# Kernel optimization log

Hardware: AMD Instinct MI355X
Metric: run time of the kernel (lower is better)

The kernel has to match this reference:

```python
import jax, jax.numpy as jnp
import numpy as np

N_NODES = 19385
N_EDGES = 1_200_000
GNN = 256
HID = 512
RANK = 512
NCLS = 3
NGENES = 6640
NBLK = 6
B = 256
EPS = 1e-5


def _ln(x, g, b):
    m = jnp.mean(x, axis=-1, keepdims=True)
    v = jnp.mean(jnp.square(x - m), axis=-1, keepdims=True)
    return (x - m) * jax.lax.rsqrt(v + EPS) * g + b


def setup_inputs() -> dict:
    key = jax.random.key(0)
    ks = iter(jax.random.split(key, 40))
    w = lambda shape, s=0.02: jax.random.normal(next(ks), shape, jnp.float32) * s
    inp = {
        'node_idx': jax.random.randint(next(ks), (B,), -1, N_NODES),  # -1 == OOV
        'edge_index': jax.random.randint(next(ks), (2, N_EDGES), 0, N_NODES),
        'edge_weight': jax.random.uniform(next(ks), (N_EDGES,), jnp.float32),
        'frozen_emb': jax.random.normal(next(ks), (N_NODES, GNN), jnp.float32),
        # trainable partial GNN (mps.6, mps.7, post_mp)
        'conv6_W': w((GNN, GNN)), 'conv6_b': jnp.zeros((GNN,)),
        'ln6_g': jnp.ones((GNN,)), 'ln6_b': jnp.zeros((GNN,)),
        'conv7_W': w((GNN, GNN)), 'conv7_b': jnp.zeros((GNN,)),
        'ln7_g': jnp.ones((GNN,)), 'ln7_b': jnp.zeros((GNN,)),
        'post_W': w((GNN, GNN)), 'post_b': jnp.zeros((GNN,)),
        # head
        'oov_emb': w((GNN,)),
        'in_ln_g': jnp.ones((GNN,)), 'in_ln_b': jnp.zeros((GNN,)),
        'proj_in_W': w((GNN, HID)), 'proj_in_b': jnp.zeros((HID,)),
        'rb_ln_g': jnp.ones((NBLK, HID)), 'rb_ln_b': jnp.zeros((NBLK, HID)),
        'rb_W1': w((NBLK, HID, 4 * HID)), 'rb_b1': jnp.zeros((NBLK, 4 * HID)),
        'rb_W2': w((NBLK, 4 * HID, HID)), 'rb_b2': jnp.zeros((NBLK, HID)),
        'out_ln_g': jnp.ones((HID,)), 'out_ln_b': jnp.zeros((HID,)),
        'bil_W': w((HID, NCLS * RANK)), 'bil_b': jnp.zeros((NCLS * RANK,)),
        'out_gene_emb': w((NGENES, RANK)),
    }
    return inp


def reference(node_idx, edge_index, edge_weight, frozen_emb,
              conv6_W, conv6_b, ln6_g, ln6_b,
              conv7_W, conv7_b, ln7_g, ln7_b,
              post_W, post_b,
              oov_emb, in_ln_g, in_ln_b, proj_in_W, proj_in_b,
              rb_ln_g, rb_ln_b, rb_W1, rb_b1, rb_W2, rb_b2,
              out_ln_g, out_ln_b, bil_W, bil_b, out_gene_emb):
    src, dst = edge_index[0], edge_index[1]

    def conv(x, W, b):
        # edge-weighted message passing: gather -> scale -> scatter-add -> linear
        msg = x[src] * edge_weight[:, None]              # [E, GNN]
        agg = jax.ops.segment_sum(msg, dst, num_segments=N_NODES)
        return agg @ W + b

    # trainable GNN layers (eval mode: dropout = identity)
    x = frozen_emb
    x = x + jax.nn.relu(_ln(conv(x, conv6_W, conv6_b), ln6_g, ln6_b))
    x = x + jax.nn.relu(_ln(conv(x, conv7_W, conv7_b), ln7_g, ln7_b))
    node_emb = x @ post_W + post_b                       # [N, GNN]

    # OOV-aware lookup
    in_f = (node_idx >= 0).astype(jnp.float32)[:, None]  # [B,1]
    gnn_emb = node_emb[jnp.clip(node_idx, 0, None)]      # [B, GNN]
    h = gnn_emb * in_f + oov_emb[None, :] * (1.0 - in_f)

    # MLP head
    h = _ln(h, in_ln_g, in_ln_b) @ proj_in_W + proj_in_b
    for i in range(NBLK):
        t = _ln(h, rb_ln_g[i], rb_ln_b[i])
        t = jax.nn.gelu(t @ rb_W1[i] + rb_b1[i])
        h = h + t @ rb_W2[i] + rb_b2[i]
    h = _ln(h, out_ln_g, out_ln_b)

    pert = (h @ bil_W + bil_b).reshape(B, NCLS, RANK)
    logits = jnp.einsum('bcr,gr->bcg', pert, out_gene_emb)  # [B, 3, 6640]
    return logits
```

## Files before the change

### kernel.cpp

```cpp
#include <hip/hip_runtime.h>
#include <hip/hip_bf16.h>
#include <cstdint>
#include <cstddef>

#define N_NODES_C 19385
#define N_EDGES_C 1200000
#define GNN_C 256
#define HID_C 512
#define RANK_C 512
#define NCLS_C 3
#define NGENES_C 6640
#define NBLK_C 6
#define B_C 256
#define LN_EPS 1e-5f

typedef short bf8v __attribute__((ext_vector_type(8)));
typedef float f4v __attribute__((ext_vector_type(4)));

__device__ __forceinline__ float bfu2f(unsigned short u) {
  union { unsigned int i; float f; } c; c.i = ((unsigned)u) << 16; return c.f;
}
__device__ __forceinline__ unsigned short f2bfu(float v) {
  union { float f; unsigned u; } c; c.f = v;
  unsigned r = c.u + 0x7FFFu + ((c.u >> 16) & 1u);
  return (unsigned short)(r >> 16);
}
__device__ __forceinline__ float gelu_tanh(float v) {
  const float x3 = v * v * v;
  return 0.5f * v * (1.f + tanhf(0.7978845608028654f * (v + 0.044715f * x3)));
}


struct CvtSeg { const float* s; unsigned short* d; long long n; };
struct CvtArgs { CvtSeg seg[2]; int nseg; };

__global__ __launch_bounds__(256) void multicvt_kernel(CvtArgs a) {
  for (int sg = 0; sg < a.nseg; ++sg) {
    const float4* s = reinterpret_cast<const float4*>(a.seg[sg].s);
    unsigned short* d = a.seg[sg].d;
    const long long n4 = a.seg[sg].n >> 2;
    for (long long i = blockIdx.x * 256 + threadIdx.x; i < n4;
         i += (long long)gridDim.x * 256) {
      float4 v = s[i];
      ushort4 o;
      o.x = f2bfu(v.x); o.y = f2bfu(v.y); o.z = f2bfu(v.z); o.w = f2bfu(v.w);
      *reinterpret_cast<ushort4*>(d + i * 4) = o;
    }
  }
}


struct TSeg { const float* s; unsigned short* d; int R, C; };
struct TArgs { TSeg seg[12]; int nseg; };

__global__ __launch_bounds__(256) void multitrans_kernel(TArgs a) {
  __shared__ float tile[32][33];
  const int tx = threadIdx.x & 31;
  const int ty = threadIdx.x >> 5;
  for (int sg = 0; sg < a.nseg; ++sg) {
    const int R = a.seg[sg].R, C = a.seg[sg].C;
    const int tC = C >> 5;
    const int nt = (R >> 5) * tC;
    const float* src = a.seg[sg].s;
    unsigned short* dst = a.seg[sg].d;
    for (int tid = blockIdx.x; tid < nt; tid += gridDim.x) {
      const int tr = tid / tC, tc = tid - tr * tC;
      const int r0 = tr * 32, c0 = tc * 32;
      __syncthreads();
#pragma unroll
      for (int j = 0; j < 32; j += 8)
        tile[ty + j][tx] = src[(size_t)(r0 + ty + j) * C + c0 + tx];
      __syncthreads();
#pragma unroll
      for (int j = 0; j < 32; j += 8)
        dst[(size_t)(c0 + ty + j) * R + r0 + tx] = f2bfu(tile[tx][ty + j]);
    }
  }
}


__global__ __launch_bounds__(256) void hist_kernel(const int* __restrict__ dst,
                                                   int* __restrict__ cnt, int E) {
  int i = blockIdx.x * 256 + threadIdx.x;
  if (i < E) atomicAdd(&cnt[dst[i]], 1);
}

__global__ __launch_bounds__(1024) void scan_kernel(const int* __restrict__ cnt,
                                                    int* __restrict__ off, int n) {
  __shared__ int sums[1024];
  const int t = threadIdx.x;
  const int CH = (n + 1023) >> 10;
  const int base = t * CH;
  int s = 0;
  for (int i = 0; i < CH; ++i) {
    int idx = base + i;
    if (idx < n) s += cnt[idx];
  }
  sums[t] = s;
  __syncthreads();
  for (int d = 1; d < 1024; d <<= 1) {
    int v = (t >= d) ? sums[t - d] : 0;
    __syncthreads();
    sums[t] += v;
    __syncthreads();
  }
  int run = (t == 0) ? 0 : sums[t - 1];
  for (int i = 0; i < CH; ++i) {
    int idx = base + i;
    if (idx < n) { off[idx] = run; run += cnt[idx]; }
  }
  if (t == 0) off[n] = sums[1023];
}

__global__ __launch_bounds__(256) void fill_kernel(const int* __restrict__ src,
                                                   const int* __restrict__ dst,
                                                   const float* __restrict__ ew,
                                                   const int* __restrict__ off,
                                                   int* __restrict__ cur,
                                                   int* __restrict__ bsrc,
                                                   float* __restrict__ bw, int E) {
  int i = blockIdx.x * 256 + threadIdx.x;
  if (i < E) {
    int d = dst[i];
    int p = atomicAdd(&cur[d], 1);
    int q = off[d] + p;
    bsrc[q] = src[i] * GNN_C;
    bw[q] = ew[i];
  }
}

__global__ __launch_bounds__(256) void mark_kernel(const int* __restrict__ node_idx,
                                                   const int* __restrict__ off,
                                                   const int* __restrict__ bsrc,
                                                   int* __restrict__ needed) {
  const int b = blockIdx.x;
  const int n = max(node_idx[b], 0);
  if (threadIdx.x == 0) needed[n] = 1;
  const int s0 = off[n], s1 = off[n + 1];
  for (int p = s0 + threadIdx.x; p < s1; p += 256)
    needed[bsrc[p] >> 8] = 1;
}


__global__ __launch_bounds__(256) void agg_full_kernel(const int* __restrict__ bsrc,
                                                       const float* __restrict__ bw,
                                                       const int* __restrict__ off,
                                                       const int* __restrict__ needed,
                                                       const unsigned short* __restrict__ x,
                                                       unsigned short* __restrict__ aggbf) {
  const int n = blockIdx.x;
  if (!needed[n]) return;
  __shared__ f4v red[4][64];
  const int t = threadIdx.x;
  const int w = __builtin_amdgcn_readfirstlane(t >> 6);
  const int lane = t & 63;
  const int s0 = off[n];
  const int c = off[n + 1] - s0;
  const int q0 = s0 + ((c * w) >> 2);
  const int q1 = s0 + ((c * (w + 1)) >> 2);
  float a0 = 0.f, a1 = 0.f, a2 = 0.f, a3 = 0.f;
  const unsigned short* xl = x + 4 * lane;
#pragma unroll 4
  for (int p = q0; p < q1; ++p) {
    const int s = bsrc[p];
    const float wg = bw[p];
    const ushort4 v = *reinterpret_cast<const ushort4*>(xl + s);
    a0 = fmaf(bfu2f(v.x), wg, a0);
    a1 = fmaf(bfu2f(v.y), wg, a1);
    a2 = fmaf(bfu2f(v.z), wg, a2);
    a3 = fmaf(bfu2f(v.w), wg, a3);
  }
  f4v av; av[0] = a0; av[1] = a1; av[2] = a2; av[3] = a3;
  red[w][lane] = av;
  __syncthreads();
  const float* rf = reinterpret_cast<const float*>(red);
  const float sum = rf[t] + rf[256 + t] + rf[512 + t] + rf[768 + t];
  aggbf[(size_t)n * GNN_C + t] = f2bfu(sum);
}

__global__ __launch_bounds__(256) void agg_sel_kernel(const int* __restrict__ node_idx,
                                                      const int* __restrict__ bsrc,
                                                      const float* __restrict__ bw,
                                                      const int* __restrict__ off,
                                                      const float* __restrict__ x,
                                                      unsigned short* __restrict__ aggbf) {
  __shared__ f4v red[4][64];
  const int b = blockIdx.x;
  const int t = threadIdx.x;
  const int n = max(node_idx[b], 0);
  const int w = __builtin_amdgcn_readfirstlane(t >> 6);
  const int lane = t & 63;
  const int s0 = off[n];
  const int c = off[n + 1] - s0;
  const int q0 = s0 + ((c * w) >> 2);
  const int q1 = s0 + ((c * (w + 1)) >> 2);
  float a0 = 0.f, a1 = 0.f, a2 = 0.f, a3 = 0.f;
  const float* xl = x + 4 * lane;
#pragma unroll 2
  for (int p = q0; p < q1; ++p) {
    const int s = bsrc[p];
    const float wg = bw[p];
    const f4v v = *reinterpret_cast<const f4v*>(xl + s);
    a0 = fmaf(v[0], wg, a0);
    a1 = fmaf(v[1], wg, a1);
    a2 = fmaf(v[2], wg, a2);
    a3 = fmaf(v[3], wg, a3);
  }
  f4v av; av[0] = a0; av[1] = a1; av[2] = a2; av[3] = a3;
  red[w][lane] = av;
  __syncthreads();
  const float* rf = reinterpret_cast<const float*>(red);
  const float sum = rf[t] + rf[256 + t] + rf[512 + t] + rf[768 + t];
  aggbf[(size_t)b * GNN_C + t] = f2bfu(sum);
}


#define MBK 32
#define MLDW 40

__global__ __launch_bounds__(256) void mgemm_kernel(const unsigned short* __restrict__ A,
                                                    const unsigned short* __restrict__ Bt,
                                                    const float* __restrict__ bias,
                                                    float* __restrict__ C,
                                                    int M, int N, int K) {
  __shared__ unsigned short As[128][MLDW];
  __shared__ unsigned short Bs[128][MLDW];
  const int t = threadIdx.x;
  const int lane = t & 63;
  const int wave = t >> 6;
  const int r0 = blockIdx.x * 128;
  const int c0 = blockIdx.y * 128;
  const int wm = (wave >> 1) * 64;
  const int wn = (wave & 1) * 64;
  const int lm = lane & 15;
  const int lq = lane >> 4;

  f4v acc[4][4];
  for (int i = 0; i < 4; ++i)
    for (int j = 0; j < 4; ++j)
      for (int r = 0; r < 4; ++r) acc[i][j][r] = 0.f;

  const int row = t >> 1;
  const int kof = (t & 1) * 16;
  for (int k0 = 0; k0 < K; k0 += MBK) {
    {
      const int gr = r0 + row;
      uint4 u0 = make_uint4(0, 0, 0, 0), u1 = u0;
      if (gr < M) {
        const uint4* p = reinterpret_cast<const uint4*>(A + (size_t)gr * K + k0 + kof);
        u0 = p[0]; u1 = p[1];
      }
      *reinterpret_cast<uint4*>(&As[row][kof]) = u0;
      *reinterpret_cast<uint4*>(&As[row][kof + 8]) = u1;
    }
    {
      const int gn = c0 + row;
      uint4 u0 = make_uint4(0, 0, 0, 0), u1 = u0;
      if (gn < N) {
        const uint4* p = reinterpret_cast<const uint4*>(Bt + (size_t)gn * K + k0 + kof);
        u0 = p[0]; u1 = p[1];
      }
      *reinterpret_cast<uint4*>(&Bs[row][kof]) = u0;
      *reinterpret_cast<uint4*>(&Bs[row][kof + 8]) = u1;
    }
    __syncthreads();

    bf8v a[4], b[4];
#pragma unroll
    for (int i = 0; i < 4; ++i)
      a[i] = *reinterpret_cast<const bf8v*>(&As[wm + i * 16 + lm][lq * 8]);
#pragma unroll
    for (int j = 0; j < 4; ++j)
      b[j] = *reinterpret_cast<const bf8v*>(&Bs[wn + j * 16 + lm][lq * 8]);
#pragma unroll
    for (int i = 0; i < 4; ++i)
#pragma unroll
      for (int j = 0; j < 4; ++j)
        acc[i][j] = __builtin_amdgcn_mfma_f32_16x16x32_bf16(a[i], b[j], acc[i][j], 0, 0, 0);
    __syncthreads();
  }

  for (int ti = 0; ti < 4; ++ti) {
    for (int tj = 0; tj < 4; ++tj) {
      const int col = c0 + wn + tj * 16 + lm;
      if (col >= N) continue;
      const float bv = bias ? bias[col] : 0.f;
      for (int r = 0; r < 4; ++r) {
        const int row2 = r0 + wm + ti * 16 + lq * 4 + r;
        if (row2 < M) C[(size_t)row2 * N + col] = acc[ti][tj][r] + bv;
      }
    }
  }
}


__global__ __launch_bounds__(256) void mgemm64_kernel(const unsigned short* __restrict__ A,
                                                      const unsigned short* __restrict__ Bt,
                                                      const float* __restrict__ bias,
                                                      float* outF, unsigned short* outB,
                                                      int M, int N, int K, int doGelu) {
  __shared__ unsigned short As[64][MLDW];
  __shared__ unsigned short Bs[64][MLDW];
  const int t = threadIdx.x;
  const int lane = t & 63;
  const int wave = t >> 6;
  const int r0 = blockIdx.x * 64;
  const int c0 = blockIdx.y * 64;
  const int wm = (wave >> 1) * 32;
  const int wn = (wave & 1) * 32;
  const int lm = lane & 15;
  const int lq = lane >> 4;

  f4v acc[2][2];
  for (int i = 0; i < 2; ++i)
    for (int j = 0; j < 2; ++j)
      for (int r = 0; r < 4; ++r) acc[i][j][r] = 0.f;

  const int row = t >> 2;
  const int kof = (t & 3) * 8;
  for (int k0 = 0; k0 < K; k0 += MBK) {
    *reinterpret_cast<uint4*>(&As[row][kof]) =
        *reinterpret_cast<const uint4*>(A + (size_t)(r0 + row) * K + k0 + kof);
    *reinterpret_cast<uint4*>(&Bs[row][kof]) =
        *reinterpret_cast<const uint4*>(Bt + (size_t)(c0 + row) * K + k0 + kof);
    __syncthreads();
    bf8v a[2], b[2];
#pragma unroll
    for (int i = 0; i < 2; ++i)
      a[i] = *reinterpret_cast<const bf8v*>(&As[wm + i * 16 + lm][lq * 8]);
#pragma unroll
    for (int j = 0; j < 2; ++j)
      b[j] = *reinterpret_cast<const bf8v*>(&Bs[wn + j * 16 + lm][lq * 8]);
#pragma unroll
    for (int i = 0; i < 2; ++i)
#pragma unroll
      for (int j = 0; j < 2; ++j)
        acc[i][j] = __builtin_amdgcn_mfma_f32_16x16x32_bf16(a[i], b[j], acc[i][j], 0, 0, 0);
    __syncthreads();
  }

  for (int ti = 0; ti < 2; ++ti) {
    for (int tj = 0; tj < 2; ++tj) {
      const int col = c0 + wn + tj * 16 + lm;
      const float bv = bias ? bias[col] : 0.f;
      for (int r = 0; r < 4; ++r) {
        const int row2 = r0 + wm + ti * 16 + lq * 4 + r;
        float v = acc[ti][tj][r] + bv;
        if (doGelu) v = gelu_tanh(v);
        if (outF) outF[(size_t)row2 * N + col] = v;
        else outB[(size_t)row2 * N + col] = f2bfu(v);
      }
    }
  }
}

__global__ __launch_bounds__(256) void skmgemm64_kernel(const unsigned short* __restrict__ A,
                                                        const unsigned short* __restrict__ Bt,
                                                        float* __restrict__ part,
                                                        int M, int N, int K, int kc) {
  __shared__ unsigned short As[64][MLDW];
  __shared__ unsigned short Bs[64][MLDW];
  const int t = threadIdx.x;
  const int lane = t & 63;
  const int wave = t >> 6;
  const int r0 = blockIdx.x * 64;
  const int c0 = blockIdx.y * 64;
  const int kBeg = blockIdx.z * kc;
  const int kEnd = kBeg + kc;
  const int wm = (wave >> 1) * 32;
  const int wn = (wave & 1) * 32;
  const int lm = lane & 15;
  const int lq = lane >> 4;

  f4v acc[2][2];
  for (int i = 0; i < 2; ++i)
    for (int j = 0; j < 2; ++j)
      for (int r = 0; r < 4; ++r) acc[i][j][r] = 0.f;

  const int row = t >> 2;
  const int kof = (t & 3) * 8;
  for (int k0 = kBeg; k0 < kEnd; k0 += MBK) {
    *reinterpret_cast<uint4*>(&As[row][kof]) =
        *reinterpret_cast<const uint4*>(A + (size_t)(r0 + row) * K + k0 + kof);
    *reinterpret_cast<uint4*>(&Bs[row][kof]) =
        *reinterpret_cast<const uint4*>(Bt + (size_t)(c0 + row) * K + k0 + kof);
    __syncthreads();
    bf8v a[2], b[2];
#pragma unroll
    for (int i = 0; i < 2; ++i)
      a[i] = *reinterpret_cast<const bf8v*>(&As[wm + i * 16 + lm][lq * 8]);
#pragma unroll
    for (int j = 0; j < 2; ++j)
      b[j] = *reinterpret_cast<const bf8v*>(&Bs[wn + j * 16 + lm][lq * 8]);
#pragma unroll
    for (int i = 0; i < 2; ++i)
#pragma unroll
      for (int j = 0; j < 2; ++j)
        acc[i][j] = __builtin_amdgcn_mfma_f32_16x16x32_bf16(a[i], b[j], acc[i][j], 0, 0, 0);
    __syncthreads();
  }

  float* out = part + (size_t)blockIdx.z * M * N;
  for (int ti = 0; ti < 2; ++ti)
    for (int tj = 0; tj < 2; ++tj) {
      const int col = c0 + wn + tj * 16 + lm;
      for (int r = 0; r < 4; ++r) {
        const int row2 = r0 + wm + ti * 16 + lq * 4 + r;
        out[(size_t)row2 * N + col] = acc[ti][tj][r];
      }
    }
}


__global__ __launch_bounds__(256) void postconv6_kernel(const float* __restrict__ g,
                                                        const float* __restrict__ b,
                                                        const float* __restrict__ frozen,
                                                        const int* __restrict__ needed,
                                                        float* __restrict__ yx) {
  __shared__ float sb[4];
  const int n = blockIdx.x, t = threadIdx.x;
  if (!needed[n]) return;
  const float v = yx[(size_t)n * GNN_C + t];
  float s = v;
  for (int o = 32; o; o >>= 1) s += __shfl_down(s, o, 64);
  if ((t & 63) == 0) sb[t >> 6] = s;
  __syncthreads();
  const float m = (sb[0] + sb[1] + sb[2] + sb[3]) * (1.f / GNN_C);
  __syncthreads();
  const float d = v - m;
  s = d * d;
  for (int o = 32; o; o >>= 1) s += __shfl_down(s, o, 64);
  if ((t & 63) == 0) sb[t >> 6] = s;
  __syncthreads();
  const float rs = rsqrtf((sb[0] + sb[1] + sb[2] + sb[3]) * (1.f / GNN_C) + LN_EPS);
  const float xn = d * rs * g[t] + b[t];
  yx[(size_t)n * GNN_C + t] = frozen[(size_t)n * GNN_C + t] + fmaxf(xn, 0.f);
}

__global__ __launch_bounds__(256) void postconv7_kernel(const float* __restrict__ y,
                                                        const float* __restrict__ g,
                                                        const float* __restrict__ b,
                                                        const int* __restrict__ idx,
                                                        const float* __restrict__ x1f,
                                                        unsigned short* __restrict__ out) {
  __shared__ float sb[4];
  const int bi = blockIdx.x, t = threadIdx.x;
  const int n = max(idx[bi], 0);
  const float v = y[(size_t)bi * GNN_C + t];
  float s = v;
  for (int o = 32; o; o >>= 1) s += __shfl_down(s, o, 64);
  if ((t & 63) == 0) sb[t >> 6] = s;
  __syncthreads();
  const float m = (sb[0] + sb[1] + sb[2] + sb[3]) * (1.f / GNN_C);
  __syncthreads();
  const float d = v - m;
  s = d * d;
  for (int o = 32; o; o >>= 1) s += __shfl_down(s, o, 64);
  if ((t & 63) == 0) sb[t >> 6] = s;
  __syncthreads();
  const float rs = rsqrtf((sb[0] + sb[1] + sb[2] + sb[3]) * (1.f / GNN_C) + LN_EPS);
  const float xn = d * rs * g[t] + b[t];
  out[(size_t)bi * GNN_C + t] = f2bfu(x1f[(size_t)n * GNN_C + t] + fmaxf(xn, 0.f));
}

__global__ __launch_bounds__(256) void h0ln_kernel(const float* __restrict__ ne,
                                                   const int* __restrict__ idx,
                                                   const float* __restrict__ oov,
                                                   const float* __restrict__ g,
                                                   const float* __restrict__ b,
                                                   unsigned short* __restrict__ out) {
  __shared__ float sb[4];
  const int bi = blockIdx.x, t = threadIdx.x;
  const float v = (idx[bi] >= 0) ? ne[(size_t)bi * GNN_C + t] : oov[t];
  float s = v;
  for (int o = 32; o; o >>= 1) s += __shfl_down(s, o, 64);
  if ((t & 63) == 0) sb[t >> 6] = s;
  __syncthreads();
  const float m = (sb[0] + sb[1] + sb[2] + sb[3]) * (1.f / GNN_C);
  __syncthreads();
  const float d = v - m;
  s = d * d;
  for (int o = 32; o; o >>= 1) s += __shfl_down(s, o, 64);
  if ((t & 63) == 0) sb[t >> 6] = s;
  __syncthreads();
  const float rs = rsqrtf((sb[0] + sb[1] + sb[2] + sb[3]) * (1.f / GNN_C) + LN_EPS);
  out[(size_t)bi * GNN_C + t] = f2bfu(d * rs * g[t] + b[t]);
}

__global__ __launch_bounds__(256) void lnbf_kernel(const float* __restrict__ in,
                                                   const float* __restrict__ g,
                                                   const float* __restrict__ b,
                                                   unsigned short* __restrict__ out) {
  __shared__ float sb[4];
  const int r = blockIdx.x, t = threadIdx.x;
  const float v0 = in[(size_t)r * HID_C + t];
  const float v1 = in[(size_t)r * HID_C + t + 256];
  float s = v0 + v1;
  for (int o = 32; o; o >>= 1) s += __shfl_down(s, o, 64);
  if ((t & 63) == 0) sb[t >> 6] = s;
  __syncthreads();
  const float m = (sb[0] + sb[1] + sb[2] + sb[3]) * (1.f / HID_C);
  __syncthreads();
  const float d0 = v0 - m, d1 = v1 - m;
  s = d0 * d0 + d1 * d1;
  for (int o = 32; o; o >>= 1) s += __shfl_down(s, o, 64);
  if ((t & 63) == 0) sb[t >> 6] = s;
  __syncthreads();
  const float rs = rsqrtf((sb[0] + sb[1] + sb[2] + sb[3]) * (1.f / HID_C) + LN_EPS);
  out[(size_t)r * HID_C + t] = f2bfu(d0 * rs * g[t] + b[t]);
  out[(size_t)r * HID_C + t + 256] = f2bfu(d1 * rs * g[t + 256] + b[t + 256]);
}

__global__ __launch_bounds__(256) void combln_kernel(const float* __restrict__ part,
                                                     float* __restrict__ h,
                                                     const float* __restrict__ b2,
                                                     const float* __restrict__ g,
                                                     const float* __restrict__ b,
                                                     unsigned short* __restrict__ out) {
  __shared__ float sb[4];
  const int r = blockIdx.x, t = threadIdx.x;
  const int MN = B_C * HID_C;
  const size_t o0 = (size_t)r * HID_C + t;
  const size_t o1 = o0 + 256;
  float v0 = h[o0] + b2[t] + part[o0] + part[MN + o0] + part[2 * MN + o0] + part[3 * MN + o0];
  float v1 = h[o1] + b2[t + 256] + part[o1] + part[MN + o1] + part[2 * MN + o1] + part[3 * MN + o1];
  h[o0] = v0;
  h[o1] = v1;
  float s = v0 + v1;
  for (int o = 32; o; o >>= 1) s += __shfl_down(s, o, 64);
  if ((t & 63) == 0) sb[t >> 6] = s;
  __syncthreads();
  const float m = (sb[0] + sb[1] + sb[2] + sb[3]) * (1.f / HID_C);
  __syncthreads();
  const float d0 = v0 - m, d1 = v1 - m;
  s = d0 * d0 + d1 * d1;
  for (int o = 32; o; o >>= 1) s += __shfl_down(s, o, 64);
  if ((t & 63) == 0) sb[t >> 6] = s;
  __syncthreads();
  const float rs = rsqrtf((sb[0] + sb[1] + sb[2] + sb[3]) * (1.f / HID_C) + LN_EPS);
  out[o0] = f2bfu(d0 * rs * g[t] + b[t]);
  out[o1] = f2bfu(d1 * rs * g[t + 256] + b[t + 256]);
}


extern "C" void kernel_launch(void* const* d_in, const int* in_sizes, int n_in,
                              void* d_out, int out_size, void* d_ws, size_t ws_size,
                              hipStream_t stream) {
  const int* node_idx = (const int*)d_in[0];
  const int* e_src = (const int*)d_in[1];
  const int* e_dst = e_src + N_EDGES_C;
  const float* ew = (const float*)d_in[2];
  const float* frozen = (const float*)d_in[3];
  const float* W6 = (const float*)d_in[4];
  const float* b6 = (const float*)d_in[5];
  const float* g6 = (const float*)d_in[6];
  const float* bl6 = (const float*)d_in[7];
  const float* W7 = (const float*)d_in[8];
  const float* b7 = (const float*)d_in[9];
  const float* g7 = (const float*)d_in[10];
  const float* bl7 = (const float*)d_in[11];
  const float* postW = (const float*)d_in[12];
  const float* postb = (const float*)d_in[13];
  const float* oov = (const float*)d_in[14];
  const float* ing = (const float*)d_in[15];
  const float* inb = (const float*)d_in[16];
  const float* projW = (const float*)d_in[17];
  const float* projb = (const float*)d_in[18];
  const float* rbg = (const float*)d_in[19];
  const float* rbb = (const float*)d_in[20];
  const float* rbW1 = (const float*)d_in[21];
  const float* rbb1 = (const float*)d_in[22];
  const float* rbW2 = (const float*)d_in[23];
  const float* rbb2 = (const float*)d_in[24];
  const float* outg = (const float*)d_in[25];
  const float* outb = (const float*)d_in[26];
  const float* bilW = (const float*)d_in[27];
  const float* bilb = (const float*)d_in[28];
  const float* gene = (const float*)d_in[29];
  (void)in_sizes; (void)n_in; (void)out_size; (void)ws_size;

  char* ws = (char*)d_ws;
  size_t o = 0;
  auto alloc = [&](size_t bytes) -> char* {
    char* p = ws + o;
    o += (bytes + 255) & ~(size_t)255;
    return p;
  };
  int* cnt = (int*)alloc((size_t)N_NODES_C * 4);
  int* off = (int*)alloc((size_t)(N_NODES_C + 1) * 4);
  int* cur = (int*)alloc((size_t)N_NODES_C * 4);
  int* needed = (int*)alloc((size_t)N_NODES_C * 4);
  int* bsrc = (int*)alloc((size_t)N_EDGES_C * 4);
  float* bw = (float*)alloc((size_t)N_EDGES_C * 4);
  unsigned short* frozbf = (unsigned short*)alloc((size_t)N_NODES_C * GNN_C * 2);
  char* aggregion = alloc((size_t)NBLK_C * HID_C * 4 * HID_C * 2);
  unsigned short* w6t = (unsigned short*)alloc((size_t)GNN_C * GNN_C * 2);
  unsigned short* w7t = (unsigned short*)alloc((size_t)GNN_C * GNN_C * 2);
  unsigned short* postWt = (unsigned short*)alloc((size_t)GNN_C * GNN_C * 2);
  unsigned short* projWt = (unsigned short*)alloc((size_t)HID_C * GNN_C * 2);
  unsigned short* bilWt = (unsigned short*)alloc((size_t)NCLS_C * RANK_C * HID_C * 2);
  float* yx = (float*)alloc((size_t)N_NODES_C * GNN_C * 4);
  unsigned short* rbW2t = (unsigned short*)alloc((size_t)NBLK_C * 4 * HID_C * HID_C * 2);
  float* part = (float*)alloc((size_t)4 * B_C * HID_C * 4);
  unsigned short* agg7bf = (unsigned short*)alloc((size_t)B_C * GNN_C * 2);
  float* y7b = (float*)alloc((size_t)B_C * GNN_C * 4);
  unsigned short* x2bf = (unsigned short*)alloc((size_t)B_C * GNN_C * 2);
  float* nemb = (float*)alloc((size_t)B_C * GNN_C * 4);
  unsigned short* h0lbf = (unsigned short*)alloc((size_t)B_C * GNN_C * 2);
  float* h = (float*)alloc((size_t)B_C * HID_C * 4);
  unsigned short* tbf = (unsigned short*)alloc((size_t)B_C * HID_C * 2);
  unsigned short* ubf = (unsigned short*)alloc((size_t)B_C * 4 * HID_C * 2);
  unsigned short* pertbf = (unsigned short*)alloc((size_t)B_C * NCLS_C * RANK_C * 2);

  unsigned short* agg6bf = (unsigned short*)aggregion;
  unsigned short* rbW1t = (unsigned short*)aggregion;
  unsigned short* genebf = frozbf;

  (void)hipMemsetAsync(cnt, 0, (size_t)N_NODES_C * 4, stream);
  (void)hipMemsetAsync(cur, 0, (size_t)N_NODES_C * 4, stream);
  (void)hipMemsetAsync(needed, 0, (size_t)N_NODES_C * 4, stream);
  const int egrid = (N_EDGES_C + 255) / 256;
  hist_kernel<<<egrid, 256, 0, stream>>>(e_dst, cnt, N_EDGES_C);
  scan_kernel<<<1, 1024, 0, stream>>>(cnt, off, N_NODES_C);
  fill_kernel<<<egrid, 256, 0, stream>>>(e_src, e_dst, ew, off, cur, bsrc, bw, N_EDGES_C);
  mark_kernel<<<B_C, 256, 0, stream>>>(node_idx, off, bsrc, needed);

  {
    CvtArgs a;
    a.seg[0] = {frozen, frozbf, (long long)N_NODES_C * GNN_C};
    a.nseg = 1;
    multicvt_kernel<<<512, 256, 0, stream>>>(a);
  }
  {
    TArgs a;
    a.seg[0] = {W6, w6t, GNN_C, GNN_C};
    a.seg[1] = {W7, w7t, GNN_C, GNN_C};
    a.seg[2] = {postW, postWt, GNN_C, GNN_C};
    a.seg[3] = {projW, projWt, GNN_C, HID_C};
    a.seg[4] = {bilW, bilWt, HID_C, NCLS_C * RANK_C};
    a.nseg = 5;
    multitrans_kernel<<<512, 256, 0, stream>>>(a);
  }

  agg_full_kernel<<<N_NODES_C, 256, 0, stream>>>(bsrc, bw, off, needed, frozbf, agg6bf);
  {
    dim3 g((N_NODES_C + 127) / 128, GNN_C / 128);
    mgemm_kernel<<<g, 256, 0, stream>>>(agg6bf, w6t, b6, yx, N_NODES_C, GNN_C, GNN_C);
  }
  postconv6_kernel<<<N_NODES_C, 256, 0, stream>>>(g6, bl6, frozen, needed, yx);

  {
    TArgs a;
    for (int i = 0; i < NBLK_C; ++i) {
      a.seg[i] = {rbW1 + (size_t)i * HID_C * 4 * HID_C,
                  rbW1t + (size_t)i * HID_C * 4 * HID_C, HID_C, 4 * HID_C};
      a.seg[6 + i] = {rbW2 + (size_t)i * 4 * HID_C * HID_C,
                      rbW2t + (size_t)i * 4 * HID_C * HID_C, 4 * HID_C, HID_C};
    }
    a.nseg = 12;
    multitrans_kernel<<<2048, 256, 0, stream>>>(a);
  }
  {
    CvtArgs a;
    a.seg[0] = {gene, genebf, (long long)NGENES_C * RANK_C};
    a.nseg = 1;
    multicvt_kernel<<<512, 256, 0, stream>>>(a);
  }

  agg_sel_kernel<<<B_C, 256, 0, stream>>>(node_idx, bsrc, bw, off, yx, agg7bf);
  {
    dim3 g(B_C / 64, GNN_C / 64);
    mgemm64_kernel<<<g, 256, 0, stream>>>(agg7bf, w7t, b7, y7b, nullptr,
                                          B_C, GNN_C, GNN_C, 0);
  }
  postconv7_kernel<<<B_C, 256, 0, stream>>>(y7b, g7, bl7, node_idx, yx, x2bf);

  {
    dim3 g(B_C / 64, GNN_C / 64);
    mgemm64_kernel<<<g, 256, 0, stream>>>(x2bf, postWt, postb, nemb, nullptr,
                                          B_C, GNN_C, GNN_C, 0);
  }
  h0ln_kernel<<<B_C, 256, 0, stream>>>(nemb, node_idx, oov, ing, inb, h0lbf);

  {
    dim3 g(B_C / 64, HID_C / 64);
    mgemm64_kernel<<<g, 256, 0, stream>>>(h0lbf, projWt, projb, h, nullptr,
                                          B_C, HID_C, GNN_C, 0);
  }
  lnbf_kernel<<<B_C, 256, 0, stream>>>(h, rbg, rbb, tbf);

  for (int i = 0; i < NBLK_C; ++i) {
    {
      dim3 g(B_C / 64, (4 * HID_C) / 64);
      mgemm64_kernel<<<g, 256, 0, stream>>>(tbf, rbW1t + (size_t)i * HID_C * 4 * HID_C,
                                            rbb1 + (size_t)i * 4 * HID_C, nullptr, ubf,
                                            B_C, 4 * HID_C, HID_C, 1);
    }
    {
      dim3 g(B_C / 64, HID_C / 64, 4);
      skmgemm64_kernel<<<g, 256, 0, stream>>>(ubf, rbW2t + (size_t)i * 4 * HID_C * HID_C,
                                              part, B_C, HID_C, 4 * HID_C, HID_C);
    }
    const float* gn = (i < NBLK_C - 1) ? rbg + (size_t)(i + 1) * HID_C : outg;
    const float* bn = (i < NBLK_C - 1) ? rbb + (size_t)(i + 1) * HID_C : outb;
    combln_kernel<<<B_C, 256, 0, stream>>>(part, h, rbb2 + (size_t)i * HID_C, gn, bn, tbf);
  }

  {
    dim3 g(B_C / 64, (NCLS_C * RANK_C) / 64);
    mgemm64_kernel<<<g, 256, 0, stream>>>(tbf, bilWt, bilb, nullptr, pertbf,
                                          B_C, NCLS_C * RANK_C, HID_C, 0);
  }

  {
    dim3 g((B_C * NCLS_C) / 128, (NGENES_C + 127) / 128);
    mgemm_kernel<<<g, 256, 0, stream>>>(pertbf, genebf, nullptr, (float*)d_out,
                                        B_C * NCLS_C, NGENES_C, RANK_C);
  }
}
```

Before: 655.7 us.

## Build CSR only for needed destinations with packed edge pairs and partitioned fill

Computes the set of needed nodes (batch nodes plus their in-neighbours) before building the CSR. Histogram and fill then skip edges whose destination is not needed. Source index and weight are packed into one 8-byte record, and the fill kernel splits destinations into 8 ranges per block team to localize atomics and scattered writes. This adds a full extra pass over the edge list, and each fill team rescans all edges.

```diff
diff --git a/kernel.cpp b/kernel.cpp
--- a/kernel.cpp
+++ b/kernel.cpp
@@ -16,6 +16,7 @@
 
 typedef short bf8v __attribute__((ext_vector_type(8)));
 typedef float f4v __attribute__((ext_vector_type(4)));
+typedef int i2v __attribute__((ext_vector_type(2)));
 
 __device__ __forceinline__ float bfu2f(unsigned short u) {
   union { unsigned int i; float f; } c; c.i = ((unsigned)u) << 16; return c.f;
@@ -79,10 +80,32 @@
 }
 
 
+__global__ __launch_bounds__(256) void marksel_kernel(const int* __restrict__ node_idx,
+                                                      int* __restrict__ selbm,
+                                                      int* __restrict__ needed) {
+  const int b = threadIdx.x;
+  const int n = max(node_idx[b], 0);
+  selbm[n] = 1;
+  needed[n] = 1;
+}
+
+__global__ __launch_bounds__(256) void marksrc_kernel(const int* __restrict__ src,
+                                                      const int* __restrict__ dst,
+                                                      const int* __restrict__ selbm,
+                                                      int* __restrict__ needed, int E) {
+  const int i = blockIdx.x * 256 + threadIdx.x;
+  if (i < E && selbm[dst[i]]) needed[src[i]] = 1;
+}
+
+
 __global__ __launch_bounds__(256) void hist_kernel(const int* __restrict__ dst,
+                                                   const int* __restrict__ needed,
                                                    int* __restrict__ cnt, int E) {
   int i = blockIdx.x * 256 + threadIdx.x;
-  if (i < E) atomicAdd(&cnt[dst[i]], 1);
+  if (i < E) {
+    const int d = dst[i];
+    if (needed[d]) atomicAdd(&cnt[d], 1);
+  }
 }
 
 __global__ __launch_bounds__(1024) void scan_kernel(const int* __restrict__ cnt,
@@ -117,33 +140,28 @@
                                                    const float* __restrict__ ew,
                                                    const int* __restrict__ off,
                                                    int* __restrict__ cur,
-                                                   int* __restrict__ bsrc,
-                                                   float* __restrict__ bw, int E) {
-  int i = blockIdx.x * 256 + threadIdx.x;
-  if (i < E) {
-    int d = dst[i];
-    int p = atomicAdd(&cur[d], 1);
-    int q = off[d] + p;
-    bsrc[q] = src[i] * GNN_C;
-    bw[q] = ew[i];
-  }
-}
-
-__global__ __launch_bounds__(256) void mark_kernel(const int* __restrict__ node_idx,
-                                                   const int* __restrict__ off,
-                                                   const int* __restrict__ bsrc,
-                                                   int* __restrict__ needed) {
-  const int b = blockIdx.x;
-  const int n = max(node_idx[b], 0);
-  if (threadIdx.x == 0) needed[n] = 1;
-  const int s0 = off[n], s1 = off[n + 1];
-  for (int p = s0 + threadIdx.x; p < s1; p += 256)
-    needed[bsrc[p] >> 8] = 1;
-}
-
-
-__global__ __launch_bounds__(256) void agg_full_kernel(const int* __restrict__ bsrc,
-                                                       const float* __restrict__ bw,
+                                                   const int* __restrict__ needed,
+                                                   i2v* __restrict__ ep, int E) {
+  const int CHN = (N_NODES_C + 7) / 8;
+  const int team = blockIdx.x & 7;
+  const int nlo = team * CHN;
+  const int nhi = min(nlo + CHN, N_NODES_C);
+  const int nb = gridDim.x >> 3;
+  const int step = nb * 256;
+  for (int i = (blockIdx.x >> 3) * 256 + threadIdx.x; i < E; i += step) {
+    const int d = dst[i];
+    if (d < nlo || d >= nhi) continue;
+    if (!needed[d]) continue;
+    const int p = atomicAdd(&cur[d], 1);
+    i2v e;
+    e[0] = src[i] * GNN_C;
+    e[1] = __float_as_int(ew[i]);
+    ep[off[d] + p] = e;
+  }
+}
+
+
+__global__ __launch_bounds__(256) void agg_full_kernel(const i2v* __restrict__ ep,
                                                        const int* __restrict__ off,
                                                        const int* __restrict__ needed,
                                                        const unsigned short* __restrict__ x,
@@ -162,8 +180,9 @@
   const unsigned short* xl = x + 4 * lane;
 #pragma unroll 4
   for (int p = q0; p < q1; ++p) {
-    const int s = bsrc[p];
-    const float wg = bw[p];
+    const i2v e = ep[p];
+    const int s = e[0];
+    const float wg = __int_as_float(e[1]);
     const ushort4 v = *reinterpret_cast<const ushort4*>(xl + s);
     a0 = fmaf(bfu2f(v.x), wg, a0);
     a1 = fmaf(bfu2f(v.y), wg, a1);
@@ -179,8 +198,7 @@
 }
 
 __global__ __launch_bounds__(256) void agg_sel_kernel(const int* __restrict__ node_idx,
-                                                      const int* __restrict__ bsrc,
-                                                      const float* __restrict__ bw,
+                                                      const i2v* __restrict__ ep,
                                                       const int* __restrict__ off,
                                                       const float* __restrict__ x,
                                                       unsigned short* __restrict__ aggbf) {
@@ -198,8 +216,9 @@
   const float* xl = x + 4 * lane;
 #pragma unroll 2
   for (int p = q0; p < q1; ++p) {
-    const int s = bsrc[p];
-    const float wg = bw[p];
+    const i2v e = ep[p];
+    const int s = e[0];
+    const float wg = __int_as_float(e[1]);
     const f4v v = *reinterpret_cast<const f4v*>(xl + s);
     a0 = fmaf(v[0], wg, a0);
     a1 = fmaf(v[1], wg, a1);
@@ -590,8 +609,8 @@
   int* off = (int*)alloc((size_t)(N_NODES_C + 1) * 4);
   int* cur = (int*)alloc((size_t)N_NODES_C * 4);
   int* needed = (int*)alloc((size_t)N_NODES_C * 4);
-  int* bsrc = (int*)alloc((size_t)N_EDGES_C * 4);
-  float* bw = (float*)alloc((size_t)N_EDGES_C * 4);
+  int* selbm = (int*)alloc((size_t)N_NODES_C * 4);
+  i2v* ep = (i2v*)alloc((size_t)N_EDGES_C * 8);
   unsigned short* frozbf = (unsigned short*)alloc((size_t)N_NODES_C * GNN_C * 2);
   char* aggregion = alloc((size_t)NBLK_C * HID_C * 4 * HID_C * 2);
   unsigned short* w6t = (unsigned short*)alloc((size_t)GNN_C * GNN_C * 2);
@@ -619,11 +638,13 @@
   (void)hipMemsetAsync(cnt, 0, (size_t)N_NODES_C * 4, stream);
   (void)hipMemsetAsync(cur, 0, (size_t)N_NODES_C * 4, stream);
   (void)hipMemsetAsync(needed, 0, (size_t)N_NODES_C * 4, stream);
+  (void)hipMemsetAsync(selbm, 0, (size_t)N_NODES_C * 4, stream);
   const int egrid = (N_EDGES_C + 255) / 256;
-  hist_kernel<<<egrid, 256, 0, stream>>>(e_dst, cnt, N_EDGES_C);
+  marksel_kernel<<<1, 256, 0, stream>>>(node_idx, selbm, needed);
+  marksrc_kernel<<<egrid, 256, 0, stream>>>(e_src, e_dst, selbm, needed, N_EDGES_C);
+  hist_kernel<<<egrid, 256, 0, stream>>>(e_dst, needed, cnt, N_EDGES_C);
   scan_kernel<<<1, 1024, 0, stream>>>(cnt, off, N_NODES_C);
-  fill_kernel<<<egrid, 256, 0, stream>>>(e_src, e_dst, ew, off, cur, bsrc, bw, N_EDGES_C);
-  mark_kernel<<<B_C, 256, 0, stream>>>(node_idx, off, bsrc, needed);
+  fill_kernel<<<512, 256, 0, stream>>>(e_src, e_dst, ew, off, cur, needed, ep, N_EDGES_C);
 
   {
     CvtArgs a;
@@ -642,7 +663,7 @@
     multitrans_kernel<<<512, 256, 0, stream>>>(a);
   }
 
-  agg_full_kernel<<<N_NODES_C, 256, 0, stream>>>(bsrc, bw, off, needed, frozbf, agg6bf);
+  agg_full_kernel<<<N_NODES_C, 256, 0, stream>>>(ep, off, needed, frozbf, agg6bf);
   {
     dim3 g((N_NODES_C + 127) / 128, GNN_C / 128);
     mgemm_kernel<<<g, 256, 0, stream>>>(agg6bf, w6t, b6, yx, N_NODES_C, GNN_C, GNN_C);
@@ -667,7 +688,7 @@
     multicvt_kernel<<<512, 256, 0, stream>>>(a);
   }
 
-  agg_sel_kernel<<<B_C, 256, 0, stream>>>(node_idx, bsrc, bw, off, yx, agg7bf);
+  agg_sel_kernel<<<B_C, 256, 0, stream>>>(node_idx, ep, off, yx, agg7bf);
   {
     dim3 g(B_C / 64, GNN_C / 64);
     mgemm64_kernel<<<g, 256, 0, stream>>>(agg7bf, w7t, b7, y7b, nullptr,
```

After: 655.6 us. About the same (-0.0%).
